# Performance work log

Measured on AMD Instinct MI355X. Metric: run time of the kernel, lower is better.

## Reference

```python
import jax, jax.numpy as jnp
import numpy as np

L, B, D_IN, H, N, NUM_LAYERS = 2048, 16, 64, 512, 64, 4


def setup_inputs() -> dict:
    key = jax.random.key(0)
    ks = jax.random.split(key, 9)
    x = jax.random.normal(ks[0], (L, B, D_IN), dtype=jnp.float32)
    enc_W = jax.random.normal(ks[1], (D_IN, H), dtype=jnp.float32) / np.sqrt(D_IN)
    enc_b = jax.random.normal(ks[2], (H,), dtype=jnp.float32) * 0.01
    # Per-layer S4D parameters, stacked along leading layer axis.
    log_dt = jax.random.uniform(ks[3], (NUM_LAYERS, H), dtype=jnp.float32,
                                minval=np.log(1e-3), maxval=np.log(1e-1))
    log_A_re = jnp.log(0.5 * jnp.ones((NUM_LAYERS, H, N), dtype=jnp.float32))
    A_im = jnp.broadcast_to(np.pi * jnp.arange(N, dtype=jnp.float32),
                            (NUM_LAYERS, H, N)).copy()
    C_re = jax.random.normal(ks[4], (NUM_LAYERS, H, N), dtype=jnp.float32)
    C_im = jax.random.normal(ks[5], (NUM_LAYERS, H, N), dtype=jnp.float32)
    Dskip = jax.random.normal(ks[6], (NUM_LAYERS, H), dtype=jnp.float32)
    return {"x": x, "enc_W": enc_W, "enc_b": enc_b, "log_dt": log_dt,
            "log_A_re": log_A_re, "A_im": A_im, "C_re": C_re, "C_im": C_im,
            "Dskip": Dskip}


def _s4d_layer(u, log_dt, log_A_re, A_im, C_re, C_im, Dskip):
    """u: [L,B,H] real. Diagonal SSM recurrent scan (ZOH discretization)."""
    dt = jnp.exp(log_dt)[:, None]                      # [H,1]
    A = -jnp.exp(log_A_re) + 1j * A_im                 # [H,N] complex, Re<0
    dA = jnp.exp(dt * A)                               # [H,N]
    dB = (dA - 1.0) / A                                # [H,N]
    C = (C_re + 1j * C_im).astype(jnp.complex64)       # [H,N]

    def step(s, u_t):                                  # s:[B,H,N] c64, u_t:[B,H]
        s = dA * s + dB * u_t[..., None]
        y = 2.0 * jnp.einsum('hn,bhn->bh', C, s).real + Dskip * u_t
        return s, y.astype(u_t.dtype)

    s0 = jnp.zeros((u.shape[1], u.shape[2], A.shape[-1]), dtype=jnp.complex64)
    sT, ys = jax.lax.scan(step, s0, u)
    return ys, sT


def reference(x, enc_W, enc_b, log_dt, log_A_re, A_im, C_re, C_im, Dskip):
    # batch_first=False: x is [L,B,D_IN]; torch code transposes to [B,L,·],
    # applies encoder, runs layers, transposes back -> equivalent to keeping
    # time-major [L,B,H] throughout.
    h = x @ enc_W + enc_b                              # [L,B,H]
    states_re, states_im = [], []
    for i in range(NUM_LAYERS):
        h, sT = _s4d_layer(h, log_dt[i], log_A_re[i], A_im[i],
                           C_re[i], C_im[i], Dskip[i])
        states_re.append(sT.real)
        states_im.append(sT.imag)
    return h, jnp.stack(states_re), jnp.stack(states_im)
```

## Files before the change

kernel.cpp:

```cpp
#include <hip/hip_runtime.h>
#include <math.h>

#define L_SEQ 2048
#define B_SZ 16
#define DIN 64
#define H_SZ 512
#define N_ST 64
#define N_LAYERS 4
#define Q_CHUNK 64
#define N_CHUNKS (L_SEQ / Q_CHUNK)
#define GSZ 4
#define N_GROUPS (N_CHUNKS / GSZ)
#define UPAD 2056
#define NTHR 768

typedef _Float16 f16;
typedef _Float16 f16x8 __attribute__((ext_vector_type(8)));
typedef _Float16 f16x4 __attribute__((ext_vector_type(4)));
typedef float    f32x4 __attribute__((ext_vector_type(4)));

struct cx { float r, i; };
__device__ __forceinline__ cx cmul(cx a, cx b) {
    return { a.r * b.r - a.i * b.i, a.r * b.i + a.i * b.r };
}

__device__ __forceinline__ void barrier_lgkm() {
    asm volatile("s_waitcnt lgkmcnt(0)\n\ts_barrier" ::: "memory");
}

__global__ __launch_bounds__(256, 4)
void encoder_mfma_kernel(const float* __restrict__ x, const float* __restrict__ W,
                         const float* __restrict__ bias, f16* __restrict__ out)
{
    __shared__ f16   x_sh[64][72];
    __shared__ f16   w_t[64][72];
    __shared__ float out_sh[64][68];
    __shared__ float b_sh[64];
    const int tid = threadIdx.x;
    const int bid = blockIdx.x;
    const int bb  = bid & 15;
    const int lt  = (bid >> 4) & 31;
    const int ht  = bid >> 9;
    const int l0 = lt * 64, h0 = ht * 64;

#pragma unroll
    for (int i = 0; i < 16; ++i) {
        int idx = tid + i * 256;
        int r = idx >> 6, c = idx & 63;
        x_sh[r][c] = (f16)x[((size_t)(l0 + r) * B_SZ + bb) * DIN + c];
        w_t[c][r]  = (f16)W[(size_t)r * H_SZ + h0 + c];
    }
    if (tid < 64) b_sh[tid] = bias[h0 + tid];
    __syncthreads();

    const int wave = tid >> 6;
    const int lane = tid & 63;
    const int frow = lane & 15;
    const int fk   = (lane >> 4) * 8;
    const int m0   = wave * 16;

    f16x8 a0 = *(const f16x8*)&w_t[m0 + frow][fk];
    f16x8 a1 = *(const f16x8*)&w_t[m0 + frow][fk + 32];
    float bv[4];
#pragma unroll
    for (int j = 0; j < 4; ++j) bv[j] = b_sh[m0 + (lane >> 4) * 4 + j];

#pragma unroll
    for (int nt = 0; nt < 4; ++nt) {
        f16x8 b0 = *(const f16x8*)&x_sh[nt * 16 + frow][fk];
        f16x8 b1 = *(const f16x8*)&x_sh[nt * 16 + frow][fk + 32];
        f32x4 acc = {0.f, 0.f, 0.f, 0.f};
        acc = __builtin_amdgcn_mfma_f32_16x16x32_f16(a0, b0, acc, 0, 0, 0);
        acc = __builtin_amdgcn_mfma_f32_16x16x32_f16(a1, b1, acc, 0, 0, 0);
#pragma unroll
        for (int j = 0; j < 4; ++j)
            out_sh[m0 + (lane >> 4) * 4 + j][nt * 16 + frow] = acc[j] + bv[j];
    }
    __syncthreads();

#pragma unroll
    for (int i = 0; i < 4; ++i) {
        int row = (tid >> 4) + i * 16;
        int c4  = (tid & 15) * 4;
        f32x4 v = *(const f32x4*)&out_sh[row][c4];
        f16x4 o;
#pragma unroll
        for (int k = 0; k < 4; ++k) o[k] = (f16)v[k];
        *(f16x4*)&out[((size_t)(h0 + row) * B_SZ + bb) * L_SEQ + l0 + c4] = o;
    }
}

__global__ __launch_bounds__(NTHR, 3)
void s4d_fused_kernel(f16* __restrict__ u_io,
                      const float* __restrict__ log_dt, const float* __restrict__ log_A_re,
                      const float* __restrict__ A_im, const float* __restrict__ C_re,
                      const float* __restrict__ C_im, const float* __restrict__ Dskip,
                      float* __restrict__ st_re, float* __restrict__ st_im)
{
    __shared__ f16   A_lds[192][72];
    __shared__ f16   G_lds[65][136];
    __shared__ f16   U_all[16][UPAD];
    __shared__ f16   S_buf[2][GSZ][16][136];
    __shared__ float dBv_sh[128];
    __shared__ float K_sh[64];
    __shared__ float w_sh[64][2];

    const int tid  = threadIdx.x;
    const int wave = tid >> 6;
    const int lane = tid & 63;
    const int h    = blockIdx.x;
    const int frow = lane & 15;
    const int fq   = lane >> 4;
    const int fk   = fq * 8;

    {
        const f16* ub = u_io + (size_t)h * B_SZ * L_SEQ;
        for (int u0 = tid; u0 < 16 * 256; u0 += NTHR) {
            int b = u0 >> 8, cidx = (u0 & 255) * 8;
            *(f16x8*)&U_all[b][cidx] = *(const f16x8*)&ub[(size_t)b * L_SEQ + cidx];
        }
    }
    f16* yb = u_io + (size_t)h * B_SZ * L_SEQ;

    for (int layer = 0; layer < N_LAYERS; ++layer) {
        const int ph = layer * H_SZ + h;
        const int pn = ph * N_ST + lane;
        const float Dv = Dskip[ph];

        {
            float dt   = expf(log_dt[ph]);
            float Are  = -expf(log_A_re[pn]);
            float Aim  = A_im[pn];
            float mg   = expf(dt * Are);
            float phs  = dt * Aim;
            cx dA1 = { mg * cosf(phs), mg * sinf(phs) };
            float invd = 1.0f / (Are * Are + Aim * Aim);
            float nr   = dA1.r - 1.0f;
            float dBr  = (nr * Are + dA1.i * Aim) * invd;
            float dBi  = (dA1.i * Are - nr * Aim) * invd;
            float Cr   = C_re[pn];
            float Ci   = C_im[pn];
            if (wave == 0) { dBv_sh[2 * lane] = dBr; dBv_sh[2 * lane + 1] = dBi; }

            const int role = wave & 3;
            const int seg  = wave >> 2;
            cx dA2  = cmul(dA1, dA1);
            cx dA4  = cmul(dA2, dA2);
            cx dA8  = cmul(dA4, dA4);
            cx dA16 = cmul(dA8, dA8);
            cx P = { 1.f, 0.f };
            int j0 = 0, jend = 21;
            if (seg >= 1) { P = cmul(cmul(dA16, dA4), dA1); j0 = 21; jend = 42; }
            if (seg == 2) { P = cmul(P, P); j0 = 42; jend = (role >= 2) ? 65 : 64; }
            for (int j = j0; j < jend; ++j) {
                if (role == 0)      A_lds[64  + lane][63 - j] = (f16)(P.r * dBr - P.i * dBi);
                else if (role == 1) A_lds[128 + lane][63 - j] = (f16)(P.r * dBi + P.i * dBr);
                else if (role == 2) G_lds[j][2 * lane]     = (f16)( 2.f * (Cr * P.r - Ci * P.i));
                else {
                    G_lds[j][2 * lane + 1] = (f16)(-2.f * (Cr * P.i + Ci * P.r));
                    if (j == 64) { w_sh[lane][0] = P.r; w_sh[lane][1] = P.i; }
                }
                P = cmul(P, dA1);
            }
        }
        barrier_lgkm();

        if (tid < 512) {
            const int t  = tid >> 3;
            const int l8 = tid & 7;
            f16x8 g0 = *(const f16x8*)&G_lds[t][l8 * 16];
            f16x8 g1 = *(const f16x8*)&G_lds[t][l8 * 16 + 8];
            f32x4 d0 = *(const f32x4*)&dBv_sh[l8 * 16];
            f32x4 d1 = *(const f32x4*)&dBv_sh[l8 * 16 + 4];
            f32x4 d2 = *(const f32x4*)&dBv_sh[l8 * 16 + 8];
            f32x4 d3 = *(const f32x4*)&dBv_sh[l8 * 16 + 12];
            float acc = 0.f;
#pragma unroll
            for (int k = 0; k < 4; ++k) {
                acc += (float)g0[k]     * d0[k];
                acc += (float)g0[k + 4] * d1[k];
                acc += (float)g1[k]     * d2[k];
                acc += (float)g1[k + 4] * d3[k];
            }
            acc += __shfl_xor(acc, 1);
            acc += __shfl_xor(acc, 2);
            acc += __shfl_xor(acc, 4);
            if (l8 == 0) K_sh[t] = acc;
        }
        barrier_lgkm();
        for (int e = tid; e < 64 * 64; e += NTHR) {
            int i = e >> 6, jc = e & 63;
            A_lds[i][jc] = (jc < i) ? (f16)K_sh[i - jc]
                         : (jc == i ? (f16)(K_sh[0] + Dv) : (f16)0.f);
        }
        barrier_lgkm();

        f16x8 aRe0, aRe1, aIm0, aIm1;
        f16x8 aT0[2], aT1[2], aG[2][4];
        float wr4[4], wi4[4];
        float s_r[4] = {0.f,0.f,0.f,0.f}, s_i[4] = {0.f,0.f,0.f,0.f};
        if (wave < 4) {
            const int m0 = 16 * wave;
            aRe0 = *(const f16x8*)&A_lds[64  + m0 + frow][fk];
            aRe1 = *(const f16x8*)&A_lds[64  + m0 + frow][fk + 32];
            aIm0 = *(const f16x8*)&A_lds[128 + m0 + frow][fk];
            aIm1 = *(const f16x8*)&A_lds[128 + m0 + frow][fk + 32];
#pragma unroll
            for (int p = 0; p < 4; ++p) {
                int n = m0 + fq * 4 + p;
                wr4[p] = w_sh[n][0]; wi4[p] = w_sh[n][1];
            }
        } else {
            const int mh = (wave - 4) & 1;
#pragma unroll
            for (int mt = 0; mt < 2; ++mt) {
                const int r0 = 32 * mh + 16 * mt + frow;
                aT0[mt] = *(const f16x8*)&A_lds[r0][fk];
                aT1[mt] = *(const f16x8*)&A_lds[r0][fk + 32];
#pragma unroll
                for (int k4 = 0; k4 < 4; ++k4)
                    aG[mt][k4] = *(const f16x8*)&G_lds[1 + r0][fk + 32 * k4];
            }
        }
        f16x4 yh[2];

        for (int g = 0; g <= N_GROUPS + 1; ++g) {
            if (wave < 4) {
                if (g < N_GROUPS) {
                    const int gb = g & 1;
#pragma unroll
                    for (int j = 0; j < GSZ; ++j) {
                        f16x8 sf;
                        sf[0] = (f16)s_r[0]; sf[1] = (f16)s_i[0];
                        sf[2] = (f16)s_r[1]; sf[3] = (f16)s_i[1];
                        sf[4] = (f16)s_r[2]; sf[5] = (f16)s_i[2];
                        sf[6] = (f16)s_r[3]; sf[7] = (f16)s_i[3];
                        *(f16x8*)&S_buf[gb][j][frow][32 * wave + fk] = sf;
                        const int co = (g * GSZ + j) * 64;
                        f16x8 b0 = *(const f16x8*)&U_all[frow][co + fk];
                        f16x8 b1 = *(const f16x8*)&U_all[frow][co + fk + 32];
                        f32x4 aR = {0.f,0.f,0.f,0.f}, aI = {0.f,0.f,0.f,0.f};
                        aR = __builtin_amdgcn_mfma_f32_16x16x32_f16(aRe0, b0, aR, 0, 0, 0);
                        aR = __builtin_amdgcn_mfma_f32_16x16x32_f16(aRe1, b1, aR, 0, 0, 0);
                        aI = __builtin_amdgcn_mfma_f32_16x16x32_f16(aIm0, b0, aI, 0, 0, 0);
                        aI = __builtin_amdgcn_mfma_f32_16x16x32_f16(aIm1, b1, aI, 0, 0, 0);
#pragma unroll
                        for (int p = 0; p < 4; ++p) {
                            float nr2 = wr4[p] * s_r[p] - wi4[p] * s_i[p] + aR[p];
                            float ni2 = wi4[p] * s_r[p] + wr4[p] * s_i[p] + aI[p];
                            s_r[p] = nr2; s_i[p] = ni2;
                        }
                    }
                }
            } else {
                const int ow = wave - 4, jc = ow >> 1, mh = ow & 1;
                if (layer < N_LAYERS - 1 && g >= 2) {
                    const int co2 = ((g - 2) * GSZ + jc) * 64;
                    *(f16x4*)&U_all[frow][co2 + 32 * mh + fq * 4]      = yh[0];
                    *(f16x4*)&U_all[frow][co2 + 32 * mh + 16 + fq * 4] = yh[1];
                }
                if (g >= 1 && g <= N_GROUPS) {
                    const int gp = g - 1, pb = gp & 1;
                    const int co = (gp * GSZ + jc) * 64;
                    f16x8 b0 = *(const f16x8*)&U_all[frow][co + fk];
                    f16x8 b1 = *(const f16x8*)&U_all[frow][co + fk + 32];
                    f16x8 sv0 = *(const f16x8*)&S_buf[pb][jc][frow][fk];
                    f16x8 sv1 = *(const f16x8*)&S_buf[pb][jc][frow][fk + 32];
                    f16x8 sv2 = *(const f16x8*)&S_buf[pb][jc][frow][fk + 64];
                    f16x8 sv3 = *(const f16x8*)&S_buf[pb][jc][frow][fk + 96];
#pragma unroll
                    for (int mt = 0; mt < 2; ++mt) {
                        f32x4 acc = {0.f,0.f,0.f,0.f};
                        acc = __builtin_amdgcn_mfma_f32_16x16x32_f16(aT0[mt], b0, acc, 0, 0, 0);
                        acc = __builtin_amdgcn_mfma_f32_16x16x32_f16(aT1[mt], b1, acc, 0, 0, 0);
                        acc = __builtin_amdgcn_mfma_f32_16x16x32_f16(aG[mt][0], sv0, acc, 0, 0, 0);
                        acc = __builtin_amdgcn_mfma_f32_16x16x32_f16(aG[mt][1], sv1, acc, 0, 0, 0);
                        acc = __builtin_amdgcn_mfma_f32_16x16x32_f16(aG[mt][2], sv2, acc, 0, 0, 0);
                        acc = __builtin_amdgcn_mfma_f32_16x16x32_f16(aG[mt][3], sv3, acc, 0, 0, 0);
                        const int t0 = 32 * mh + 16 * mt + fq * 4;
                        f16x4 o;
#pragma unroll
                        for (int k = 0; k < 4; ++k) o[k] = (f16)acc[k];
                        if (layer == N_LAYERS - 1)
                            *(f16x4*)&yb[(size_t)frow * L_SEQ + co + t0] = o;
                        else
                            yh[mt] = o;
                    }
                }
            }
            barrier_lgkm();
        }

        if (wave < 4) {
#pragma unroll
            for (int p = 0; p < 4; ++p) {
                int n = 16 * wave + 4 * fq + p;
                size_t base = (((size_t)layer * B_SZ + frow) * H_SZ + h) * N_ST + n;
                st_re[base] = s_r[p];
                st_im[base] = s_i[p];
            }
        }
        __syncthreads();
    }
}

__global__ __launch_bounds__(256, 4)
void hbl_to_lbh_kernel(const f16* __restrict__ in, float* __restrict__ out)
{
    __shared__ float t_sh[64][65];
    const int tid = threadIdx.x, bid = blockIdx.x;
    const int bb = bid & 15, lt = (bid >> 4) & 31, ht = bid >> 9;
    const int l0 = lt * 64, h0 = ht * 64;
#pragma unroll
    for (int i = 0; i < 4; ++i) {
        int idx = tid + i * 256;
        int hh = idx >> 4, l4 = (idx & 15) * 4;
        f16x4 v = *(const f16x4*)&in[((size_t)(h0 + hh) * B_SZ + bb) * L_SEQ + l0 + l4];
#pragma unroll
        for (int k = 0; k < 4; ++k) t_sh[hh][l4 + k] = (float)v[k];
    }
    __syncthreads();
#pragma unroll
    for (int i = 0; i < 4; ++i) {
        int idx = tid + i * 256;
        int ll = idx >> 4, h4 = (idx & 15) * 4;
        float4 o = make_float4(t_sh[h4][ll], t_sh[h4 + 1][ll],
                               t_sh[h4 + 2][ll], t_sh[h4 + 3][ll]);
        *(float4*)&out[((size_t)(l0 + ll) * B_SZ + bb) * H_SZ + h0 + h4] = o;
    }
}

extern "C" void kernel_launch(void* const* d_in, const int* in_sizes, int n_in,
                              void* d_out, int out_size, void* d_ws, size_t ws_size,
                              hipStream_t stream)
{
    const float* x        = (const float*)d_in[0];
    const float* enc_W    = (const float*)d_in[1];
    const float* enc_b    = (const float*)d_in[2];
    const float* log_dt   = (const float*)d_in[3];
    const float* log_A_re = (const float*)d_in[4];
    const float* A_im     = (const float*)d_in[5];
    const float* C_re     = (const float*)d_in[6];
    const float* C_im     = (const float*)d_in[7];
    const float* Dskip    = (const float*)d_in[8];

    float* out_lbh = (float*)d_out;
    float* st_re   = out_lbh + (size_t)L_SEQ * B_SZ * H_SZ;
    float* st_im   = st_re + (size_t)N_LAYERS * B_SZ * H_SZ * N_ST;
    f16*   B0      = (f16*)d_ws;

    encoder_mfma_kernel<<<4096, 256, 0, stream>>>(x, enc_W, enc_b, B0);

    s4d_fused_kernel<<<512, NTHR, 0, stream>>>(B0, log_dt, log_A_re, A_im,
                                               C_re, C_im, Dskip, st_re, st_im);

    hbl_to_lbh_kernel<<<4096, 256, 0, stream>>>(B0, out_lbh);
}
```

Measured before the change: 242.9 us.

## Overlap next-layer SSM parameter setup with the tail of the chunk pipeline

Layer-parameter setup (dA/dB powers, G matrix, K kernel, Toeplitz matrix) now runs only up front for layer 0. For later layers it is done by the state-recurrence waves during the idle pipeline-drain iterations of the previous layer, and the Toeplitz rebuild happens after the loop. This hides per-layer setup and removes several block-wide barriers. The risk is that it relies on those waves being idle at those group indices and on LDS regions not being read concurrently. The encoder load is also vectorized to float4 reads.

```diff
diff --git a/kernel.cpp b/kernel.cpp
--- a/kernel.cpp
+++ b/kernel.cpp
@@ -44,11 +44,18 @@
     const int l0 = lt * 64, h0 = ht * 64;
 
 #pragma unroll
-    for (int i = 0; i < 16; ++i) {
-        int idx = tid + i * 256;
-        int r = idx >> 6, c = idx & 63;
-        x_sh[r][c] = (f16)x[((size_t)(l0 + r) * B_SZ + bb) * DIN + c];
-        w_t[c][r]  = (f16)W[(size_t)r * H_SZ + h0 + c];
+    for (int i = 0; i < 4; ++i) {
+        int e  = tid + i * 256;
+        int r  = e >> 4;
+        int c4 = (e & 15) * 4;
+        float4 xv = *(const float4*)&x[((size_t)(l0 + r) * B_SZ + bb) * DIN + c4];
+        f16x4 xo; xo[0] = (f16)xv.x; xo[1] = (f16)xv.y; xo[2] = (f16)xv.z; xo[3] = (f16)xv.w;
+        *(f16x4*)&x_sh[r][c4] = xo;
+        float4 wv = *(const float4*)&W[(size_t)r * H_SZ + h0 + c4];
+        w_t[c4 + 0][r] = (f16)wv.x;
+        w_t[c4 + 1][r] = (f16)wv.y;
+        w_t[c4 + 2][r] = (f16)wv.z;
+        w_t[c4 + 3][r] = (f16)wv.w;
     }
     if (tid < 64) b_sh[tid] = bias[h0 + tid];
     __syncthreads();
@@ -127,73 +134,74 @@
         const int pn = ph * N_ST + lane;
         const float Dv = Dskip[ph];
 
-        {
-            float dt   = expf(log_dt[ph]);
-            float Are  = -expf(log_A_re[pn]);
-            float Aim  = A_im[pn];
-            float mg   = expf(dt * Are);
-            float phs  = dt * Aim;
-            cx dA1 = { mg * cosf(phs), mg * sinf(phs) };
-            float invd = 1.0f / (Are * Are + Aim * Aim);
-            float nr   = dA1.r - 1.0f;
-            float dBr  = (nr * Are + dA1.i * Aim) * invd;
-            float dBi  = (dA1.i * Are - nr * Aim) * invd;
-            float Cr   = C_re[pn];
-            float Ci   = C_im[pn];
-            if (wave == 0) { dBv_sh[2 * lane] = dBr; dBv_sh[2 * lane + 1] = dBi; }
-
-            const int role = wave & 3;
-            const int seg  = wave >> 2;
-            cx dA2  = cmul(dA1, dA1);
-            cx dA4  = cmul(dA2, dA2);
-            cx dA8  = cmul(dA4, dA4);
-            cx dA16 = cmul(dA8, dA8);
-            cx P = { 1.f, 0.f };
-            int j0 = 0, jend = 21;
-            if (seg >= 1) { P = cmul(cmul(dA16, dA4), dA1); j0 = 21; jend = 42; }
-            if (seg == 2) { P = cmul(P, P); j0 = 42; jend = (role >= 2) ? 65 : 64; }
-            for (int j = j0; j < jend; ++j) {
-                if (role == 0)      A_lds[64  + lane][63 - j] = (f16)(P.r * dBr - P.i * dBi);
-                else if (role == 1) A_lds[128 + lane][63 - j] = (f16)(P.r * dBi + P.i * dBr);
-                else if (role == 2) G_lds[j][2 * lane]     = (f16)( 2.f * (Cr * P.r - Ci * P.i));
-                else {
-                    G_lds[j][2 * lane + 1] = (f16)(-2.f * (Cr * P.i + Ci * P.r));
-                    if (j == 64) { w_sh[lane][0] = P.r; w_sh[lane][1] = P.i; }
+        if (layer == 0) {
+            {
+                float dt   = expf(log_dt[ph]);
+                float Are  = -expf(log_A_re[pn]);
+                float Aim  = A_im[pn];
+                float mg   = expf(dt * Are);
+                float phs  = dt * Aim;
+                cx dA1 = { mg * cosf(phs), mg * sinf(phs) };
+                float invd = 1.0f / (Are * Are + Aim * Aim);
+                float nr   = dA1.r - 1.0f;
+                float dBr  = (nr * Are + dA1.i * Aim) * invd;
+                float dBi  = (dA1.i * Are - nr * Aim) * invd;
+                float Cr   = C_re[pn];
+                float Ci   = C_im[pn];
+                if (wave == 0) { dBv_sh[2 * lane] = dBr; dBv_sh[2 * lane + 1] = dBi; }
+
+                const int role = wave & 3;
+                const int seg  = wave >> 2;
+                cx dA2  = cmul(dA1, dA1);
+                cx dA4  = cmul(dA2, dA2);
+                cx dA8  = cmul(dA4, dA4);
+                cx dA16 = cmul(dA8, dA8);
+                cx P = { 1.f, 0.f };
+                int j0 = 0, jend = 21;
+                if (seg >= 1) { P = cmul(cmul(dA16, dA4), dA1); j0 = 21; jend = 42; }
+                if (seg == 2) { P = cmul(P, P); j0 = 42; jend = (role >= 2) ? 65 : 64; }
+                for (int j = j0; j < jend; ++j) {
+                    if (role == 0)      A_lds[64  + lane][63 - j] = (f16)(P.r * dBr - P.i * dBi);
+                    else if (role == 1) A_lds[128 + lane][63 - j] = (f16)(P.r * dBi + P.i * dBr);
+                    else if (role == 2) G_lds[j][2 * lane]     = (f16)( 2.f * (Cr * P.r - Ci * P.i));
+                    else {
+                        G_lds[j][2 * lane + 1] = (f16)(-2.f * (Cr * P.i + Ci * P.r));
+                        if (j == 64) { w_sh[lane][0] = P.r; w_sh[lane][1] = P.i; }
+                    }
+                    P = cmul(P, dA1);
                 }
-                P = cmul(P, dA1);
-            }
-        }
-        barrier_lgkm();
-
-        if (tid < 512) {
-            const int t  = tid >> 3;
-            const int l8 = tid & 7;
-            f16x8 g0 = *(const f16x8*)&G_lds[t][l8 * 16];
-            f16x8 g1 = *(const f16x8*)&G_lds[t][l8 * 16 + 8];
-            f32x4 d0 = *(const f32x4*)&dBv_sh[l8 * 16];
-            f32x4 d1 = *(const f32x4*)&dBv_sh[l8 * 16 + 4];
-            f32x4 d2 = *(const f32x4*)&dBv_sh[l8 * 16 + 8];
-            f32x4 d3 = *(const f32x4*)&dBv_sh[l8 * 16 + 12];
-            float acc = 0.f;
-#pragma unroll
-            for (int k = 0; k < 4; ++k) {
-                acc += (float)g0[k]     * d0[k];
-                acc += (float)g0[k + 4] * d1[k];
-                acc += (float)g1[k]     * d2[k];
-                acc += (float)g1[k + 4] * d3[k];
-            }
-            acc += __shfl_xor(acc, 1);
-            acc += __shfl_xor(acc, 2);
-            acc += __shfl_xor(acc, 4);
-            if (l8 == 0) K_sh[t] = acc;
-        }
-        barrier_lgkm();
-        for (int e = tid; e < 64 * 64; e += NTHR) {
-            int i = e >> 6, jc = e & 63;
-            A_lds[i][jc] = (jc < i) ? (f16)K_sh[i - jc]
-                         : (jc == i ? (f16)(K_sh[0] + Dv) : (f16)0.f);
-        }
-        barrier_lgkm();
+            }
+            barrier_lgkm();
+            if (tid < 512) {
+                const int t  = tid >> 3;
+                const int l8 = tid & 7;
+                f16x8 g0 = *(const f16x8*)&G_lds[t][l8 * 16];
+                f16x8 g1 = *(const f16x8*)&G_lds[t][l8 * 16 + 8];
+                f32x4 d0 = *(const f32x4*)&dBv_sh[l8 * 16];
+                f32x4 d1 = *(const f32x4*)&dBv_sh[l8 * 16 + 4];
+                f32x4 d2 = *(const f32x4*)&dBv_sh[l8 * 16 + 8];
+                f32x4 d3 = *(const f32x4*)&dBv_sh[l8 * 16 + 12];
+                float acc = 0.f;
+#pragma unroll
+                for (int k = 0; k < 4; ++k) {
+                    acc += (float)g0[k]     * d0[k];
+                    acc += (float)g0[k + 4] * d1[k];
+                    acc += (float)g1[k]     * d2[k];
+                    acc += (float)g1[k + 4] * d3[k];
+                }
+                acc += __shfl_xor(acc, 1);
+                acc += __shfl_xor(acc, 2);
+                acc += __shfl_xor(acc, 4);
+                if (l8 == 0) K_sh[t] = acc;
+            }
+            barrier_lgkm();
+            for (int e = tid; e < 64 * 64; e += NTHR) {
+                int i = e >> 6, jc = e & 63;
+                A_lds[i][jc] = (jc < i) ? (f16)K_sh[i - jc]
+                             : (jc == i ? (f16)(K_sh[0] + Dv) : (f16)0.f);
+            }
+            barrier_lgkm();
+        }
 
         f16x8 aRe0, aRe1, aIm0, aIm1;
         f16x8 aT0[2], aT1[2], aG[2][4];
@@ -251,6 +259,59 @@
                             s_r[p] = nr2; s_i[p] = ni2;
                         }
                     }
+                } else if (layer < N_LAYERS - 1 && g == N_GROUPS) {
+                    const int ph2 = ph + H_SZ;
+                    const int pn2 = ph2 * N_ST + lane;
+                    float dt   = expf(log_dt[ph2]);
+                    float Are  = -expf(log_A_re[pn2]);
+                    float Aim  = A_im[pn2];
+                    float mg   = expf(dt * Are);
+                    float phs  = dt * Aim;
+                    cx dA1 = { mg * cosf(phs), mg * sinf(phs) };
+                    float invd = 1.0f / (Are * Are + Aim * Aim);
+                    float nr   = dA1.r - 1.0f;
+                    float dBr  = (nr * Are + dA1.i * Aim) * invd;
+                    float dBi  = (dA1.i * Are - nr * Aim) * invd;
+                    float Cr   = C_re[pn2];
+                    float Ci   = C_im[pn2];
+                    if (wave == 0) { dBv_sh[2 * lane] = dBr; dBv_sh[2 * lane + 1] = dBi; }
+                    cx P = { 1.f, 0.f };
+                    if (wave == 0) {
+                        for (int j = 0; j < 64; ++j) {
+                            A_lds[64 + lane][63 - j] = (f16)(P.r * dBr - P.i * dBi);
+                            P = cmul(P, dA1);
+                        }
+                    } else if (wave == 1) {
+                        for (int j = 0; j < 64; ++j) {
+                            A_lds[128 + lane][63 - j] = (f16)(P.r * dBi + P.i * dBr);
+                            P = cmul(P, dA1);
+                        }
+                    } else if (wave == 2) {
+                        for (int j = 0; j < 65; ++j) {
+                            G_lds[j][2 * lane] = (f16)( 2.f * (Cr * P.r - Ci * P.i));
+                            P = cmul(P, dA1);
+                        }
+                    } else {
+                        for (int j = 0; j < 65; ++j) {
+                            G_lds[j][2 * lane + 1] = (f16)(-2.f * (Cr * P.i + Ci * P.r));
+                            if (j == 64) { w_sh[lane][0] = P.r; w_sh[lane][1] = P.i; }
+                            P = cmul(P, dA1);
+                        }
+                    }
+                } else if (layer < N_LAYERS - 1 && g == N_GROUPS + 1) {
+                    const int t  = tid >> 2;
+                    const int l4 = tid & 3;
+                    float acc = 0.f;
+#pragma unroll
+                    for (int q = 0; q < 4; ++q) {
+                        f16x8 gv = *(const f16x8*)&G_lds[t][l4 * 32 + q * 8];
+#pragma unroll
+                        for (int k = 0; k < 8; ++k)
+                            acc += (float)gv[k] * dBv_sh[l4 * 32 + q * 8 + k];
+                    }
+                    acc += __shfl_xor(acc, 1);
+                    acc += __shfl_xor(acc, 2);
+                    if (l4 == 0) K_sh[t] = acc;
                 }
             } else {
                 const int ow = wave - 4, jc = ow >> 1, mh = ow & 1;
@@ -291,6 +352,15 @@
             barrier_lgkm();
         }
 
+        if (layer < N_LAYERS - 1) {
+            const float Dn = Dskip[ph + H_SZ];
+            for (int e = tid; e < 64 * 64; e += NTHR) {
+                int i = e >> 6, jc = e & 63;
+                A_lds[i][jc] = (jc < i) ? (f16)K_sh[i - jc]
+                             : (jc == i ? (f16)(K_sh[0] + Dn) : (f16)0.f);
+            }
+        }
+
         if (wave < 4) {
 #pragma unroll
             for (int p = 0; p < 4; ++p) {
```

New measurement: 245.4 us. No clear change (+1.0%).

## Split S4D blocks across batch halves and compute input-matrix fragments in registers

Applied to the files above, without the earlier changes.

The fused S4D kernel now launches two blocks per channel, each owning 8 of the 16 batch rows. This halves the U_all and S_buf shared memory and raises the occupancy target from 3 to 6 blocks per CU. The dB·dA^k input-matrix fragments are now computed directly in registers rather than written to and read back from LDS, which shrinks A_lds and lets the power-table work be spread over all 12 waves. The cost is that MFMA tiles are still 16 rows wide, so half of each B operand is duplicated padding and per-channel setup is repeated in both blocks. Separately, the encoder switches to float4 vectorized global loads.

```diff
diff --git a/kernel.cpp b/kernel.cpp
--- a/kernel.cpp
+++ b/kernel.cpp
@@ -13,6 +13,7 @@
 #define N_GROUPS (N_CHUNKS / GSZ)
 #define UPAD 2056
 #define NTHR 768
+#define BH 8
 
 typedef _Float16 f16;
 typedef _Float16 f16x8 __attribute__((ext_vector_type(8)));
@@ -44,11 +45,18 @@
     const int l0 = lt * 64, h0 = ht * 64;
 
 #pragma unroll
-    for (int i = 0; i < 16; ++i) {
-        int idx = tid + i * 256;
-        int r = idx >> 6, c = idx & 63;
-        x_sh[r][c] = (f16)x[((size_t)(l0 + r) * B_SZ + bb) * DIN + c];
-        w_t[c][r]  = (f16)W[(size_t)r * H_SZ + h0 + c];
+    for (int i = 0; i < 4; ++i) {
+        int e  = tid + i * 256;
+        int r  = e >> 4;
+        int c4 = (e & 15) * 4;
+        float4 xv = *(const float4*)&x[((size_t)(l0 + r) * B_SZ + bb) * DIN + c4];
+        f16x4 xo; xo[0] = (f16)xv.x; xo[1] = (f16)xv.y; xo[2] = (f16)xv.z; xo[3] = (f16)xv.w;
+        *(f16x4*)&x_sh[r][c4] = xo;
+        float4 wv = *(const float4*)&W[(size_t)r * H_SZ + h0 + c4];
+        w_t[c4 + 0][r] = (f16)wv.x;
+        w_t[c4 + 1][r] = (f16)wv.y;
+        w_t[c4 + 2][r] = (f16)wv.z;
+        w_t[c4 + 3][r] = (f16)wv.w;
     }
     if (tid < 64) b_sh[tid] = bias[h0 + tid];
     __syncthreads();
@@ -90,17 +98,17 @@
     }
 }
 
-__global__ __launch_bounds__(NTHR, 3)
+__global__ __launch_bounds__(NTHR, 6)
 void s4d_fused_kernel(f16* __restrict__ u_io,
                       const float* __restrict__ log_dt, const float* __restrict__ log_A_re,
                       const float* __restrict__ A_im, const float* __restrict__ C_re,
                       const float* __restrict__ C_im, const float* __restrict__ Dskip,
                       float* __restrict__ st_re, float* __restrict__ st_im)
 {
-    __shared__ f16   A_lds[192][72];
+    __shared__ f16   A_lds[64][72];
     __shared__ f16   G_lds[65][136];
-    __shared__ f16   U_all[16][UPAD];
-    __shared__ f16   S_buf[2][GSZ][16][136];
+    __shared__ f16   U_all[BH][UPAD];
+    __shared__ f16   S_buf[2][GSZ][BH][136];
     __shared__ float dBv_sh[128];
     __shared__ float K_sh[64];
     __shared__ float w_sh[64][2];
@@ -108,24 +116,31 @@
     const int tid  = threadIdx.x;
     const int wave = tid >> 6;
     const int lane = tid & 63;
-    const int h    = blockIdx.x;
+    const int h    = blockIdx.x >> 1;
+    const int bh   = blockIdx.x & 1;
     const int frow = lane & 15;
     const int fq   = lane >> 4;
     const int fk   = fq * 8;
+    const int fr8  = frow & 7;
 
     {
-        const f16* ub = u_io + (size_t)h * B_SZ * L_SEQ;
-        for (int u0 = tid; u0 < 16 * 256; u0 += NTHR) {
+        const f16* ub = u_io + ((size_t)h * B_SZ + bh * BH) * L_SEQ;
+        for (int u0 = tid; u0 < BH * 256; u0 += NTHR) {
             int b = u0 >> 8, cidx = (u0 & 255) * 8;
             *(f16x8*)&U_all[b][cidx] = *(const f16x8*)&ub[(size_t)b * L_SEQ + cidx];
         }
     }
-    f16* yb = u_io + (size_t)h * B_SZ * L_SEQ;
+    f16* yb = u_io + ((size_t)h * B_SZ + bh * BH) * L_SEQ;
 
     for (int layer = 0; layer < N_LAYERS; ++layer) {
         const int ph = layer * H_SZ + h;
         const int pn = ph * N_ST + lane;
         const float Dv = Dskip[ph];
+
+        f16x8 aRe0, aRe1, aIm0, aIm1;
+        f16x8 aT0[2], aT1[2], aG[2][4];
+        float wr4[4], wi4[4];
+        float s_r[4] = {0.f,0.f,0.f,0.f}, s_i[4] = {0.f,0.f,0.f,0.f};
 
         {
             float dt   = expf(log_dt[ph]);
@@ -142,25 +157,65 @@
             float Ci   = C_im[pn];
             if (wave == 0) { dBv_sh[2 * lane] = dBr; dBv_sh[2 * lane + 1] = dBi; }
 
-            const int role = wave & 3;
-            const int seg  = wave >> 2;
-            cx dA2  = cmul(dA1, dA1);
-            cx dA4  = cmul(dA2, dA2);
-            cx dA8  = cmul(dA4, dA4);
-            cx dA16 = cmul(dA8, dA8);
+            const int role = wave & 1;
+            const int seg  = wave >> 1;
+            cx d2  = cmul(dA1, dA1);
+            cx d4  = cmul(d2, d2);
+            cx d8  = cmul(d4, d4);
+            cx d11 = cmul(cmul(d8, d2), dA1);
+            cx d22 = cmul(d11, d11);
+            cx d44 = cmul(d22, d22);
             cx P = { 1.f, 0.f };
-            int j0 = 0, jend = 21;
-            if (seg >= 1) { P = cmul(cmul(dA16, dA4), dA1); j0 = 21; jend = 42; }
-            if (seg == 2) { P = cmul(P, P); j0 = 42; jend = (role >= 2) ? 65 : 64; }
+            if (seg & 1) P = cmul(P, d11);
+            if (seg & 2) P = cmul(P, d22);
+            if (seg & 4) P = cmul(P, d44);
+            const int j0 = 11 * seg;
+            const int jend = (j0 + 11 < 65) ? (j0 + 11) : 65;
             for (int j = j0; j < jend; ++j) {
-                if (role == 0)      A_lds[64  + lane][63 - j] = (f16)(P.r * dBr - P.i * dBi);
-                else if (role == 1) A_lds[128 + lane][63 - j] = (f16)(P.r * dBi + P.i * dBr);
-                else if (role == 2) G_lds[j][2 * lane]     = (f16)( 2.f * (Cr * P.r - Ci * P.i));
+                if (role == 0) G_lds[j][2 * lane]     = (f16)( 2.f * (Cr * P.r - Ci * P.i));
                 else {
                     G_lds[j][2 * lane + 1] = (f16)(-2.f * (Cr * P.i + Ci * P.r));
                     if (j == 64) { w_sh[lane][0] = P.r; w_sh[lane][1] = P.i; }
                 }
                 P = cmul(P, dA1);
+            }
+
+            if (wave < 4) {
+                const int nf  = 16 * wave + frow;
+                const int pnf = ph * N_ST + nf;
+                float AreF = -expf(log_A_re[pnf]);
+                float AimF = A_im[pnf];
+                float mgF  = expf(dt * AreF);
+                float phF  = dt * AimF;
+                cx dAf = { mgF * cosf(phF), mgF * sinf(phF) };
+                float invF = 1.0f / (AreF * AreF + AimF * AimF);
+                float nrF  = dAf.r - 1.0f;
+                float dBrF = (nrF * AreF + dAf.i * AimF) * invF;
+                float dBiF = (dAf.i * AreF - nrF * AimF) * invF;
+                cx f2  = cmul(dAf, dAf);
+                cx f4  = cmul(f2, f2);
+                cx f8  = cmul(f4, f4);
+                cx f16p = cmul(f8, f8);
+                cx f32p = cmul(f16p, f16p);
+                cx one = { 1.f, 0.f };
+                cx Pa = f32p;
+                Pa = cmul(Pa, (fq < 2) ? f16p : one);
+                Pa = cmul(Pa, ((fq & 1) == 0) ? f8 : one);
+#pragma unroll
+                for (int q = 7; q >= 0; --q) {
+                    aRe0[q] = (f16)(Pa.r * dBrF - Pa.i * dBiF);
+                    aIm0[q] = (f16)(Pa.r * dBiF + Pa.i * dBrF);
+                    Pa = cmul(Pa, dAf);
+                }
+                cx Pb = one;
+                Pb = cmul(Pb, (fq < 2) ? f16p : one);
+                Pb = cmul(Pb, ((fq & 1) == 0) ? f8 : one);
+#pragma unroll
+                for (int q = 7; q >= 0; --q) {
+                    aRe1[q] = (f16)(Pb.r * dBrF - Pb.i * dBiF);
+                    aIm1[q] = (f16)(Pb.r * dBiF + Pb.i * dBrF);
+                    Pb = cmul(Pb, dAf);
+                }
             }
         }
         barrier_lgkm();
@@ -172,14 +227,14 @@
             f16x8 g1 = *(const f16x8*)&G_lds[t][l8 * 16 + 8];
             f32x4 d0 = *(const f32x4*)&dBv_sh[l8 * 16];
             f32x4 d1 = *(const f32x4*)&dBv_sh[l8 * 16 + 4];
-            f32x4 d2 = *(const f32x4*)&dBv_sh[l8 * 16 + 8];
+            f32x4 d2v = *(const f32x4*)&dBv_sh[l8 * 16 + 8];
             f32x4 d3 = *(const f32x4*)&dBv_sh[l8 * 16 + 12];
             float acc = 0.f;
 #pragma unroll
             for (int k = 0; k < 4; ++k) {
                 acc += (float)g0[k]     * d0[k];
                 acc += (float)g0[k + 4] * d1[k];
-                acc += (float)g1[k]     * d2[k];
+                acc += (float)g1[k]     * d2v[k];
                 acc += (float)g1[k + 4] * d3[k];
             }
             acc += __shfl_xor(acc, 1);
@@ -188,6 +243,7 @@
             if (l8 == 0) K_sh[t] = acc;
         }
         barrier_lgkm();
+
         for (int e = tid; e < 64 * 64; e += NTHR) {
             int i = e >> 6, jc = e & 63;
             A_lds[i][jc] = (jc < i) ? (f16)K_sh[i - jc]
@@ -195,16 +251,8 @@
         }
         barrier_lgkm();
 
-        f16x8 aRe0, aRe1, aIm0, aIm1;
-        f16x8 aT0[2], aT1[2], aG[2][4];
-        float wr4[4], wi4[4];
-        float s_r[4] = {0.f,0.f,0.f,0.f}, s_i[4] = {0.f,0.f,0.f,0.f};
         if (wave < 4) {
             const int m0 = 16 * wave;
-            aRe0 = *(const f16x8*)&A_lds[64  + m0 + frow][fk];
-            aRe1 = *(const f16x8*)&A_lds[64  + m0 + frow][fk + 32];
-            aIm0 = *(const f16x8*)&A_lds[128 + m0 + frow][fk];
-            aIm1 = *(const f16x8*)&A_lds[128 + m0 + frow][fk + 32];
 #pragma unroll
             for (int p = 0; p < 4; ++p) {
                 int n = m0 + fq * 4 + p;
@@ -223,6 +271,7 @@
             }
         }
         f16x4 yh[2];
+        barrier_lgkm();
 
         for (int g = 0; g <= N_GROUPS + 1; ++g) {
             if (wave < 4) {
@@ -235,10 +284,11 @@
                         sf[2] = (f16)s_r[1]; sf[3] = (f16)s_i[1];
                         sf[4] = (f16)s_r[2]; sf[5] = (f16)s_i[2];
                         sf[6] = (f16)s_r[3]; sf[7] = (f16)s_i[3];
-                        *(f16x8*)&S_buf[gb][j][frow][32 * wave + fk] = sf;
+                        if (frow < 8)
+                            *(f16x8*)&S_buf[gb][j][frow][32 * wave + fk] = sf;
                         const int co = (g * GSZ + j) * 64;
-                        f16x8 b0 = *(const f16x8*)&U_all[frow][co + fk];
-                        f16x8 b1 = *(const f16x8*)&U_all[frow][co + fk + 32];
+                        f16x8 b0 = *(const f16x8*)&U_all[fr8][co + fk];
+                        f16x8 b1 = *(const f16x8*)&U_all[fr8][co + fk + 32];
                         f32x4 aR = {0.f,0.f,0.f,0.f}, aI = {0.f,0.f,0.f,0.f};
                         aR = __builtin_amdgcn_mfma_f32_16x16x32_f16(aRe0, b0, aR, 0, 0, 0);
                         aR = __builtin_amdgcn_mfma_f32_16x16x32_f16(aRe1, b1, aR, 0, 0, 0);
@@ -254,7 +304,7 @@
                 }
             } else {
                 const int ow = wave - 4, jc = ow >> 1, mh = ow & 1;
-                if (layer < N_LAYERS - 1 && g >= 2) {
+                if (layer < N_LAYERS - 1 && g >= 2 && frow < 8) {
                     const int co2 = ((g - 2) * GSZ + jc) * 64;
                     *(f16x4*)&U_all[frow][co2 + 32 * mh + fq * 4]      = yh[0];
                     *(f16x4*)&U_all[frow][co2 + 32 * mh + 16 + fq * 4] = yh[1];
@@ -262,12 +312,12 @@
                 if (g >= 1 && g <= N_GROUPS) {
                     const int gp = g - 1, pb = gp & 1;
                     const int co = (gp * GSZ + jc) * 64;
-                    f16x8 b0 = *(const f16x8*)&U_all[frow][co + fk];
-                    f16x8 b1 = *(const f16x8*)&U_all[frow][co + fk + 32];
-                    f16x8 sv0 = *(const f16x8*)&S_buf[pb][jc][frow][fk];
-                    f16x8 sv1 = *(const f16x8*)&S_buf[pb][jc][frow][fk + 32];
-                    f16x8 sv2 = *(const f16x8*)&S_buf[pb][jc][frow][fk + 64];
-                    f16x8 sv3 = *(const f16x8*)&S_buf[pb][jc][frow][fk + 96];
+                    f16x8 b0 = *(const f16x8*)&U_all[fr8][co + fk];
+                    f16x8 b1 = *(const f16x8*)&U_all[fr8][co + fk + 32];
+                    f16x8 sv0 = *(const f16x8*)&S_buf[pb][jc][fr8][fk];
+                    f16x8 sv1 = *(const f16x8*)&S_buf[pb][jc][fr8][fk + 32];
+                    f16x8 sv2 = *(const f16x8*)&S_buf[pb][jc][fr8][fk + 64];
+                    f16x8 sv3 = *(const f16x8*)&S_buf[pb][jc][fr8][fk + 96];
 #pragma unroll
                     for (int mt = 0; mt < 2; ++mt) {
                         f32x4 acc = {0.f,0.f,0.f,0.f};
@@ -281,21 +331,23 @@
                         f16x4 o;
 #pragma unroll
                         for (int k = 0; k < 4; ++k) o[k] = (f16)acc[k];
-                        if (layer == N_LAYERS - 1)
-                            *(f16x4*)&yb[(size_t)frow * L_SEQ + co + t0] = o;
-                        else
+                        if (layer == N_LAYERS - 1) {
+                            if (frow < 8)
+                                *(f16x4*)&yb[(size_t)frow * L_SEQ + co + t0] = o;
+                        } else {
                             yh[mt] = o;
+                        }
                     }
                 }
             }
             barrier_lgkm();
         }
 
-        if (wave < 4) {
+        if (wave < 4 && frow < 8) {
 #pragma unroll
             for (int p = 0; p < 4; ++p) {
                 int n = 16 * wave + 4 * fq + p;
-                size_t base = (((size_t)layer * B_SZ + frow) * H_SZ + h) * N_ST + n;
+                size_t base = (((size_t)layer * B_SZ + bh * BH + frow) * H_SZ + h) * N_ST + n;
                 st_re[base] = s_r[p];
                 st_im[base] = s_i[p];
             }
@@ -351,8 +403,8 @@
 
     encoder_mfma_kernel<<<4096, 256, 0, stream>>>(x, enc_W, enc_b, B0);
 
-    s4d_fused_kernel<<<512, NTHR, 0, stream>>>(B0, log_dt, log_A_re, A_im,
-                                               C_re, C_im, Dskip, st_re, st_im);
+    s4d_fused_kernel<<<1024, NTHR, 0, stream>>>(B0, log_dt, log_A_re, A_im,
+                                                C_re, C_im, Dskip, st_re, st_im);
 
     hbl_to_lbh_kernel<<<4096, 256, 0, stream>>>(B0, out_lbh);
 }
```

Measured after the change: 875.5 us. 3.6x slower.

## Interleave re/im state rows, split scan over 8 waves, use 32x32 MFMA for outputs

Applied to the files above, without the earlier changes.

The A matrix now interleaves real and imaginary rows, so each of eight scan waves produces both parts of two states with one pair of 16x16 MFMAs. This halves the serial MFMA chain per step and spreads the recurrence across twice as many waves. The output waves switch to 32x32x16 MFMA tiles with per-lane operand layouts. The encoder also loads x and W as float4 vectors. The scan now uses eight waves and the output path fewer, which shifts the load balance between scan and output work and adds register pressure from the larger accumulators.

```diff
diff --git a/kernel.cpp b/kernel.cpp
--- a/kernel.cpp
+++ b/kernel.cpp
@@ -18,6 +18,7 @@
 typedef _Float16 f16x8 __attribute__((ext_vector_type(8)));
 typedef _Float16 f16x4 __attribute__((ext_vector_type(4)));
 typedef float    f32x4 __attribute__((ext_vector_type(4)));
+typedef float    f32x16 __attribute__((ext_vector_type(16)));
 
 struct cx { float r, i; };
 __device__ __forceinline__ cx cmul(cx a, cx b) {
@@ -44,11 +45,18 @@
     const int l0 = lt * 64, h0 = ht * 64;
 
 #pragma unroll
-    for (int i = 0; i < 16; ++i) {
-        int idx = tid + i * 256;
-        int r = idx >> 6, c = idx & 63;
-        x_sh[r][c] = (f16)x[((size_t)(l0 + r) * B_SZ + bb) * DIN + c];
-        w_t[c][r]  = (f16)W[(size_t)r * H_SZ + h0 + c];
+    for (int i = 0; i < 4; ++i) {
+        int e  = tid + i * 256;
+        int r  = e >> 4;
+        int c4 = (e & 15) * 4;
+        float4 xv = *(const float4*)&x[((size_t)(l0 + r) * B_SZ + bb) * DIN + c4];
+        f16x4 xo; xo[0] = (f16)xv.x; xo[1] = (f16)xv.y; xo[2] = (f16)xv.z; xo[3] = (f16)xv.w;
+        *(f16x4*)&x_sh[r][c4] = xo;
+        float4 wv = *(const float4*)&W[(size_t)r * H_SZ + h0 + c4];
+        w_t[c4 + 0][r] = (f16)wv.x;
+        w_t[c4 + 1][r] = (f16)wv.y;
+        w_t[c4 + 2][r] = (f16)wv.z;
+        w_t[c4 + 3][r] = (f16)wv.w;
     }
     if (tid < 64) b_sh[tid] = bias[h0 + tid];
     __syncthreads();
@@ -112,6 +120,10 @@
     const int frow = lane & 15;
     const int fq   = lane >> 4;
     const int fk   = fq * 8;
+    const int r32  = lane & 31;
+    const int kh   = (lane >> 5) * 8;
+    const int ch   = (lane >> 4) & 1;
+    const int thi  = (lane >> 5) * 4;
 
     {
         const f16* ub = u_io + (size_t)h * B_SZ * L_SEQ;
@@ -153,8 +165,8 @@
             if (seg >= 1) { P = cmul(cmul(dA16, dA4), dA1); j0 = 21; jend = 42; }
             if (seg == 2) { P = cmul(P, P); j0 = 42; jend = (role >= 2) ? 65 : 64; }
             for (int j = j0; j < jend; ++j) {
-                if (role == 0)      A_lds[64  + lane][63 - j] = (f16)(P.r * dBr - P.i * dBi);
-                else if (role == 1) A_lds[128 + lane][63 - j] = (f16)(P.r * dBi + P.i * dBr);
+                if (role == 0)      A_lds[64 + 2 * lane][63 - j]     = (f16)(P.r * dBr - P.i * dBi);
+                else if (role == 1) A_lds[64 + 2 * lane + 1][63 - j] = (f16)(P.r * dBi + P.i * dBr);
                 else if (role == 2) G_lds[j][2 * lane]     = (f16)( 2.f * (Cr * P.r - Ci * P.i));
                 else {
                     G_lds[j][2 * lane + 1] = (f16)(-2.f * (Cr * P.i + Ci * P.r));
@@ -195,110 +207,103 @@
         }
         barrier_lgkm();
 
-        f16x8 aRe0, aRe1, aIm0, aIm1;
-        f16x8 aT0[2], aT1[2], aG[2][4];
-        float wr4[4], wi4[4];
-        float s_r[4] = {0.f,0.f,0.f,0.f}, s_i[4] = {0.f,0.f,0.f,0.f};
-        if (wave < 4) {
-            const int m0 = 16 * wave;
-            aRe0 = *(const f16x8*)&A_lds[64  + m0 + frow][fk];
-            aRe1 = *(const f16x8*)&A_lds[64  + m0 + frow][fk + 32];
-            aIm0 = *(const f16x8*)&A_lds[128 + m0 + frow][fk];
-            aIm1 = *(const f16x8*)&A_lds[128 + m0 + frow][fk + 32];
-#pragma unroll
-            for (int p = 0; p < 4; ++p) {
-                int n = m0 + fq * 4 + p;
-                wr4[p] = w_sh[n][0]; wi4[p] = w_sh[n][1];
-            }
+        f16x8 aE0, aE1;
+        f16x8 aT[4], aG[8];
+        float war = 0.f, wai = 0.f, wbr = 0.f, wbi = 0.f;
+        float s0r = 0.f, s0i = 0.f, s1r = 0.f, s1i = 0.f;
+        if (wave < 8) {
+            aE0 = *(const f16x8*)&A_lds[64 + 16 * wave + frow][fk];
+            aE1 = *(const f16x8*)&A_lds[64 + 16 * wave + frow][fk + 32];
+            const int n0 = 8 * wave + 2 * fq;
+            war = w_sh[n0][0];     wai = w_sh[n0][1];
+            wbr = w_sh[n0 + 1][0]; wbi = w_sh[n0 + 1][1];
         } else {
-            const int mh = (wave - 4) & 1;
-#pragma unroll
-            for (int mt = 0; mt < 2; ++mt) {
-                const int r0 = 32 * mh + 16 * mt + frow;
-                aT0[mt] = *(const f16x8*)&A_lds[r0][fk];
-                aT1[mt] = *(const f16x8*)&A_lds[r0][fk + 32];
-#pragma unroll
-                for (int k4 = 0; k4 < 4; ++k4)
-                    aG[mt][k4] = *(const f16x8*)&G_lds[1 + r0][fk + 32 * k4];
-            }
-        }
-        f16x4 yh[2];
+            const int mt = (wave - 8) & 1;
+#pragma unroll
+            for (int ks = 0; ks < 4; ++ks)
+                aT[ks] = *(const f16x8*)&A_lds[32 * mt + r32][ks * 16 + kh];
+#pragma unroll
+            for (int ks = 0; ks < 8; ++ks)
+                aG[ks] = *(const f16x8*)&G_lds[1 + 32 * mt + r32][ks * 16 + kh];
+        }
+        f16x4 yh[4];
 
         for (int g = 0; g <= N_GROUPS + 1; ++g) {
-            if (wave < 4) {
+            if (wave < 8) {
                 if (g < N_GROUPS) {
                     const int gb = g & 1;
 #pragma unroll
                     for (int j = 0; j < GSZ; ++j) {
-                        f16x8 sf;
-                        sf[0] = (f16)s_r[0]; sf[1] = (f16)s_i[0];
-                        sf[2] = (f16)s_r[1]; sf[3] = (f16)s_i[1];
-                        sf[4] = (f16)s_r[2]; sf[5] = (f16)s_i[2];
-                        sf[6] = (f16)s_r[3]; sf[7] = (f16)s_i[3];
-                        *(f16x8*)&S_buf[gb][j][frow][32 * wave + fk] = sf;
+                        f16x4 sf; sf[0] = (f16)s0r; sf[1] = (f16)s0i;
+                        sf[2] = (f16)s1r; sf[3] = (f16)s1i;
+                        *(f16x4*)&S_buf[gb][j][frow][16 * wave + fq * 4] = sf;
                         const int co = (g * GSZ + j) * 64;
                         f16x8 b0 = *(const f16x8*)&U_all[frow][co + fk];
                         f16x8 b1 = *(const f16x8*)&U_all[frow][co + fk + 32];
-                        f32x4 aR = {0.f,0.f,0.f,0.f}, aI = {0.f,0.f,0.f,0.f};
-                        aR = __builtin_amdgcn_mfma_f32_16x16x32_f16(aRe0, b0, aR, 0, 0, 0);
-                        aR = __builtin_amdgcn_mfma_f32_16x16x32_f16(aRe1, b1, aR, 0, 0, 0);
-                        aI = __builtin_amdgcn_mfma_f32_16x16x32_f16(aIm0, b0, aI, 0, 0, 0);
-                        aI = __builtin_amdgcn_mfma_f32_16x16x32_f16(aIm1, b1, aI, 0, 0, 0);
-#pragma unroll
-                        for (int p = 0; p < 4; ++p) {
-                            float nr2 = wr4[p] * s_r[p] - wi4[p] * s_i[p] + aR[p];
-                            float ni2 = wi4[p] * s_r[p] + wr4[p] * s_i[p] + aI[p];
-                            s_r[p] = nr2; s_i[p] = ni2;
-                        }
+                        f32x4 acc = {0.f, 0.f, 0.f, 0.f};
+                        acc = __builtin_amdgcn_mfma_f32_16x16x32_f16(aE0, b0, acc, 0, 0, 0);
+                        acc = __builtin_amdgcn_mfma_f32_16x16x32_f16(aE1, b1, acc, 0, 0, 0);
+                        float t0r = war * s0r - wai * s0i + acc[0];
+                        float t0i = wai * s0r + war * s0i + acc[1];
+                        float t1r = wbr * s1r - wbi * s1i + acc[2];
+                        float t1i = wbi * s1r + wbr * s1i + acc[3];
+                        s0r = t0r; s0i = t0i; s1r = t1r; s1i = t1i;
                     }
                 }
             } else {
-                const int ow = wave - 4, jc = ow >> 1, mh = ow & 1;
+                const int ow = wave - 8, pp = ow >> 1, mt = ow & 1;
                 if (layer < N_LAYERS - 1 && g >= 2) {
-                    const int co2 = ((g - 2) * GSZ + jc) * 64;
-                    *(f16x4*)&U_all[frow][co2 + 32 * mh + fq * 4]      = yh[0];
-                    *(f16x4*)&U_all[frow][co2 + 32 * mh + 16 + fq * 4] = yh[1];
+                    const int co2 = ((g - 2) * GSZ + pp * 2 + ch) * 64 + 32 * mt;
+#pragma unroll
+                    for (int q = 0; q < 4; ++q)
+                        *(f16x4*)&U_all[frow][co2 + 8 * q + thi] = yh[q];
                 }
                 if (g >= 1 && g <= N_GROUPS) {
                     const int gp = g - 1, pb = gp & 1;
+                    const int jc = pp * 2 + ch;
                     const int co = (gp * GSZ + jc) * 64;
-                    f16x8 b0 = *(const f16x8*)&U_all[frow][co + fk];
-                    f16x8 b1 = *(const f16x8*)&U_all[frow][co + fk + 32];
-                    f16x8 sv0 = *(const f16x8*)&S_buf[pb][jc][frow][fk];
-                    f16x8 sv1 = *(const f16x8*)&S_buf[pb][jc][frow][fk + 32];
-                    f16x8 sv2 = *(const f16x8*)&S_buf[pb][jc][frow][fk + 64];
-                    f16x8 sv3 = *(const f16x8*)&S_buf[pb][jc][frow][fk + 96];
-#pragma unroll
-                    for (int mt = 0; mt < 2; ++mt) {
-                        f32x4 acc = {0.f,0.f,0.f,0.f};
-                        acc = __builtin_amdgcn_mfma_f32_16x16x32_f16(aT0[mt], b0, acc, 0, 0, 0);
-                        acc = __builtin_amdgcn_mfma_f32_16x16x32_f16(aT1[mt], b1, acc, 0, 0, 0);
-                        acc = __builtin_amdgcn_mfma_f32_16x16x32_f16(aG[mt][0], sv0, acc, 0, 0, 0);
-                        acc = __builtin_amdgcn_mfma_f32_16x16x32_f16(aG[mt][1], sv1, acc, 0, 0, 0);
-                        acc = __builtin_amdgcn_mfma_f32_16x16x32_f16(aG[mt][2], sv2, acc, 0, 0, 0);
-                        acc = __builtin_amdgcn_mfma_f32_16x16x32_f16(aG[mt][3], sv3, acc, 0, 0, 0);
-                        const int t0 = 32 * mh + 16 * mt + fq * 4;
-                        f16x4 o;
-#pragma unroll
-                        for (int k = 0; k < 4; ++k) o[k] = (f16)acc[k];
-                        if (layer == N_LAYERS - 1)
-                            *(f16x4*)&yb[(size_t)frow * L_SEQ + co + t0] = o;
-                        else
-                            yh[mt] = o;
+                    f16x8 bT[4], bG[8];
+#pragma unroll
+                    for (int ks = 0; ks < 4; ++ks)
+                        bT[ks] = *(const f16x8*)&U_all[frow][co + ks * 16 + kh];
+#pragma unroll
+                    for (int ks = 0; ks < 8; ++ks)
+                        bG[ks] = *(const f16x8*)&S_buf[pb][jc][frow][ks * 16 + kh];
+                    f32x16 acc = {0.f,0.f,0.f,0.f,0.f,0.f,0.f,0.f,
+                                  0.f,0.f,0.f,0.f,0.f,0.f,0.f,0.f};
+#pragma unroll
+                    for (int ks = 0; ks < 4; ++ks)
+                        acc = __builtin_amdgcn_mfma_f32_32x32x16_f16(aT[ks], bT[ks], acc, 0, 0, 0);
+#pragma unroll
+                    for (int ks = 0; ks < 8; ++ks)
+                        acc = __builtin_amdgcn_mfma_f32_32x32x16_f16(aG[ks], bG[ks], acc, 0, 0, 0);
+                    if (layer == N_LAYERS - 1) {
+#pragma unroll
+                        for (int q = 0; q < 4; ++q) {
+                            f16x4 o;
+#pragma unroll
+                            for (int k = 0; k < 4; ++k) o[k] = (f16)acc[4 * q + k];
+                            *(f16x4*)&yb[(size_t)frow * L_SEQ + co + 32 * mt + 8 * q + thi] = o;
+                        }
+                    } else {
+#pragma unroll
+                        for (int q = 0; q < 4; ++q) {
+                            f16x4 o;
+#pragma unroll
+                            for (int k = 0; k < 4; ++k) o[k] = (f16)acc[4 * q + k];
+                            yh[q] = o;
+                        }
                     }
                 }
             }
             barrier_lgkm();
         }
 
-        if (wave < 4) {
-#pragma unroll
-            for (int p = 0; p < 4; ++p) {
-                int n = 16 * wave + 4 * fq + p;
-                size_t base = (((size_t)layer * B_SZ + frow) * H_SZ + h) * N_ST + n;
-                st_re[base] = s_r[p];
-                st_im[base] = s_i[p];
-            }
+        if (wave < 8) {
+            const int na = wave * 8 + fq * 2;
+            const size_t base = (((size_t)layer * B_SZ + frow) * H_SZ + h) * N_ST + na;
+            st_re[base]     = s0r; st_im[base]     = s0i;
+            st_re[base + 1] = s1r; st_im[base + 1] = s1i;
         }
         __syncthreads();
     }
```

Result: faster. 232.7 us (-4.2%).
